# Performance work log

Hardware: AMD Instinct MI355X
Metric: run time of the kernel (lower is better)

The kernel has to match this reference:

```python
import jax, jax.numpy as jnp
import numpy as np
from jax import lax

B, C_IN, C, H, W = 4, 64, 64, 128, 128
K = 3  # window_size
SCALE = C ** (-0.5)
EPS = 1e-5  # BatchNorm eps (eval mode, running_mean=0, running_var=1)


def conv1x1(x, w, b):
    # x: (B,Ci,H,W), w: (Co,Ci)
    return jnp.einsum('bchw,oc->bohw', x, w) + b[None, :, None, None]


def unfold3(x):
    # torch nn.Unfold(kernel=3, pad=1, stride=1): (B,C,H,W) -> (B, C*9, H*W)
    b, c, h, w = x.shape
    xp = jnp.pad(x, ((0, 0), (0, 0), (1, 1), (1, 1)))
    patches = jnp.stack([xp[:, :, i:i + h, j:j + w]
                         for i in range(K) for j in range(K)], axis=2)  # (B,C,9,H,W)
    return patches.reshape(b, c * K * K, h * w)


def fold3(cols, h, w):
    # torch F.fold(kernel=3, pad=1, stride=1): (B, C*9, H*W) -> (B,C,H,W) scatter-add
    b = cols.shape[0]
    c = cols.shape[1] // (K * K)
    p = cols.reshape(b, c, K, K, h, w)
    out = jnp.zeros((b, c, h + 2, w + 2), cols.dtype)
    for i in range(K):
        for j in range(K):
            out = out.at[:, :, i:i + h, j:j + w].add(p[:, :, i, j])
    return out[:, :, 1:h + 1, 1:w + 1]


def grouped_conv3(x, w, groups):
    # 3x3 'same' conv with feature groups; w: (Cout, Cin/groups, 3, 3) OIHW
    return lax.conv_general_dilated(x, w, (1, 1), ((1, 1), (1, 1)),
                                    feature_group_count=groups,
                                    dimension_numbers=('NCHW', 'OIHW', 'NCHW'))


def bn_eval(x, g, b):
    # eval-mode BN with running_mean=0, running_var=1
    s = g / jnp.sqrt(1.0 + EPS)
    return x * s[None, :, None, None] + b[None, :, None, None]


def setup_inputs() -> dict:
    key = jax.random.key(0)
    ks = jax.random.split(key, 24)
    rn = lambda k, sh, s=1.0: (jax.random.normal(k, sh, dtype=jnp.float32) * s)
    return {
        'x':  rn(ks[0], (B, C_IN, H, W)),
        'fg': rn(ks[1], (B, C, H, W)),
        'bg': rn(ks[2], (B, C, H, W)),
        'w_x': rn(ks[3], (C, C_IN), 0.05), 'bias_x': rn(ks[4], (C,), 0.01),
        'w_f': rn(ks[5], (C, C), 0.05),    'bias_f': rn(ks[6], (C,), 0.01),
        'w_b': rn(ks[7], (C, C), 0.05),    'bias_b': rn(ks[8], (C,), 0.01),
        'w1': rn(ks[9], (C, 2, 3, 3), 0.1), 'b1': rn(ks[10], (C,), 0.01),
        'g1': jax.random.uniform(ks[11], (C,), dtype=jnp.float32, minval=0.5, maxval=1.5),
        'be1': rn(ks[12], (C,), 0.01),
        'w2': rn(ks[13], (C, C), 0.05), 'b2': rn(ks[14], (C,), 0.01),
        'w3': rn(ks[15], (C, 1, 3, 3), 0.1), 'b3': rn(ks[16], (C,), 0.01),
        'g2': jax.random.uniform(ks[17], (C,), dtype=jnp.float32, minval=0.5, maxval=1.5),
        'be2': rn(ks[18], (C,), 0.01),
        'w4': rn(ks[19], (C, C), 0.05), 'b4': rn(ks[20], (C,), 0.01),
    }


def reference(x, fg, bg, w_x, bias_x, w_f, bias_f, w_b, bias_b,
              w1, b1, g1, be1, w2, b2, w3, b3, g2, be2, w4, b4):
    b, _, h, w = x.shape
    xq  = conv1x1(x, w_x, bias_x)
    fgp = conv1x1(fg, w_f, bias_f)
    bgp = conv1x1(bg, w_b, bias_b)

    # unfold then the module's raw reshape (B, C*9, L) -> (B, C*L, 3, 3)
    xu = unfold3(xq).reshape(b, -1, K, K)
    fu = unfold3(fgp).reshape(b, -1, K, K)
    bu = unfold3(bgp).reshape(b, -1, K, K)

    attn_f = jax.nn.softmax(xu * fu, axis=-1) * xu * SCALE
    attn_b = jax.nn.softmax(xu - bu, axis=-1) * xu * SCALE

    # permute(0,2,3,1).view(B, 9*C, L) then fold back to (B,C,H,W)
    cols_f = attn_f.transpose(0, 2, 3, 1).reshape(b, K * K * C, -1)
    cols_b = attn_b.transpose(0, 2, 3, 1).reshape(b, K * K * C, -1)
    of = fold3(cols_f, h, w)
    ob = fold3(cols_b, h, w)

    a = jnp.concatenate([of, ob], axis=1)  # (B, 2C, H, W)
    y = grouped_conv3(a, w1, C) + b1[None, :, None, None]
    y = jax.nn.relu(bn_eval(y, g1, be1))
    y = conv1x1(y, w2, b2)
    y = grouped_conv3(y, w3, C) + b3[None, :, None, None]
    y = jax.nn.relu(bn_eval(y, g2, be2))
    y = conv1x1(y, w4, b4)
    return y
```

## Files before the change

### kernel.cpp

```cpp
#include <hip/hip_runtime.h>

#define NB 4
#define HWSZ 16384

typedef float f4u __attribute__((ext_vector_type(4), aligned(4)));
typedef _Float16 h8 __attribute__((ext_vector_type(8)));

#define PLANE_H ((size_t)1 << 21)

__device__ __forceinline__ void pw_body(int bid, int tid,
                                        const float* __restrict__ in,
                                        const float* __restrict__ w,
                                        const float* __restrict__ bias,
                                        float* __restrict__ out,
                                        float* wls) {
  int b = bid >> 8;
  int r = bid & 255;
  int oc = r >> 6;
  int pc = r & 63;
  int px4 = tid & 63;
  int og = tid >> 6;
  int px = (pc << 8) + (px4 << 2);
#pragma unroll
  for (int it = 0; it < 4; ++it)
    wls[(it << 8) + tid] = w[(oc << 10) + (it << 8) + tid];
  __syncthreads();
  int ob = (oc << 4) + (og << 2);
  float4 acc[4];
#pragma unroll
  for (int j = 0; j < 4; ++j) {
    float bv = bias[ob + j];
    acc[j] = make_float4(bv, bv, bv, bv);
  }
  const float* ip = in + (((size_t)b << 6) << 14) + px;
  const float* wp = wls + ((og << 2) << 6);
#pragma unroll 4
  for (int cc = 0; cc < 64; ++cc) {
    float4 xv = *(const float4*)(ip + ((size_t)cc << 14));
#pragma unroll
    for (int j = 0; j < 4; ++j) {
      float wv = wp[(j << 6) + cc];
      acc[j].x = fmaf(wv, xv.x, acc[j].x);
      acc[j].y = fmaf(wv, xv.y, acc[j].y);
      acc[j].z = fmaf(wv, xv.z, acc[j].z);
      acc[j].w = fmaf(wv, xv.w, acc[j].w);
    }
  }
#pragma unroll
  for (int j = 0; j < 4; ++j)
    *(float4*)(out + (((size_t)(b << 6) + ob + j) << 14) + px) = acc[j];
}

__global__ __launch_bounds__(256) void pw_k(const float* __restrict__ in,
                                            const float* __restrict__ w,
                                            const float* __restrict__ bias,
                                            float* __restrict__ out) {
  __shared__ float wls[16 * 64];
  pw_body(blockIdx.x, threadIdx.x, in, w, bias, out, wls);
}

__global__ __launch_bounds__(256) void pw3_k(const float* __restrict__ in0,
                                             const float* __restrict__ in1,
                                             const float* __restrict__ in2,
                                             const float* __restrict__ w0,
                                             const float* __restrict__ w1,
                                             const float* __restrict__ w2,
                                             const float* __restrict__ bi0,
                                             const float* __restrict__ bi1,
                                             const float* __restrict__ bi2,
                                             float* __restrict__ o0,
                                             float* __restrict__ o1,
                                             float* __restrict__ o2) {
  __shared__ float wls[16 * 64];
  int which = blockIdx.x >> 10;
  int bid = blockIdx.x & 1023;
  const float* in = (which == 0) ? in0 : (which == 1) ? in1 : in2;
  const float* w  = (which == 0) ? w0  : (which == 1) ? w1  : w2;
  const float* bi = (which == 0) ? bi0 : (which == 1) ? bi1 : bi2;
  float* out      = (which == 0) ? o0  : (which == 1) ? o1  : o2;
  pw_body(bid, threadIdx.x, in, w, bi, out, wls);
}

__global__ __launch_bounds__(256) void gconv1_k(const float* __restrict__ a,
                                                const float* __restrict__ w1,
                                                const float* __restrict__ b1,
                                                const float* __restrict__ g1,
                                                const float* __restrict__ be1,
                                                float* __restrict__ t1) {
  int bid = blockIdx.x;
  int b = bid >> 10;
  int r = bid & 1023;
  int o = r >> 4;
  int rc = r & 15;
  int tid = threadIdx.x;
  int px4 = tid & 31;
  int ry = tid >> 5;
  int y = (rc << 3) + ry;
  int x0 = px4 << 2;
  float bv = b1[o];
  float4 acc = make_float4(bv, bv, bv, bv);
#pragma unroll
  for (int ic = 0; ic < 2; ++ic) {
    const float* ap = a + ((size_t)(b * 128 + 2 * o + ic) << 14);
    const float* wr0 = w1 + o * 18 + ic * 9;
#pragma unroll
    for (int dy = 0; dy < 3; ++dy) {
      int yy = y + dy - 1;
      if ((unsigned)yy >= 128u) continue;
      const float* row = ap + (yy << 7);
      float4 mid = *(const float4*)(row + x0);
      float lf = (px4 > 0) ? row[x0 - 1] : 0.f;
      float rt = (px4 < 31) ? row[x0 + 4] : 0.f;
      float wa = wr0[dy * 3 + 0], wb = wr0[dy * 3 + 1], wc = wr0[dy * 3 + 2];
      acc.x += wa * lf    + wb * mid.x + wc * mid.y;
      acc.y += wa * mid.x + wb * mid.y + wc * mid.z;
      acc.z += wa * mid.y + wb * mid.z + wc * mid.w;
      acc.w += wa * mid.z + wb * mid.w + wc * rt;
    }
  }
  const float invs = 0.9999950000374997f;
  float s = g1[o] * invs, be = be1[o];
  acc.x = fmaxf(acc.x * s + be, 0.f);
  acc.y = fmaxf(acc.y * s + be, 0.f);
  acc.z = fmaxf(acc.z * s + be, 0.f);
  acc.w = fmaxf(acc.w * s + be, 0.f);
  *(float4*)(t1 + (((size_t)(b << 6) + o) << 14) + (y << 7) + x0) = acc;
}

__global__ __launch_bounds__(256) void dconv_k(const float* __restrict__ y2,
                                               const float* __restrict__ w3,
                                               const float* __restrict__ b3,
                                               const float* __restrict__ g2,
                                               const float* __restrict__ be2,
                                               float* __restrict__ t2) {
  int bid = blockIdx.x;
  int b = bid >> 10;
  int r = bid & 1023;
  int o = r >> 4;
  int rc = r & 15;
  int tid = threadIdx.x;
  int px4 = tid & 31;
  int ry = tid >> 5;
  int y = (rc << 3) + ry;
  int x0 = px4 << 2;
  float bv = b3[o];
  float4 acc = make_float4(bv, bv, bv, bv);
  const float* ap = y2 + (((size_t)(b << 6) + o) << 14);
  const float* wr0 = w3 + o * 9;
#pragma unroll
  for (int dy = 0; dy < 3; ++dy) {
    int yy = y + dy - 1;
    if ((unsigned)yy >= 128u) continue;
    const float* row = ap + (yy << 7);
    float4 mid = *(const float4*)(row + x0);
    float lf = (px4 > 0) ? row[x0 - 1] : 0.f;
    float rt = (px4 < 31) ? row[x0 + 4] : 0.f;
    float wa = wr0[dy * 3 + 0], wb = wr0[dy * 3 + 1], wc = wr0[dy * 3 + 2];
    acc.x += wa * lf    + wb * mid.x + wc * mid.y;
    acc.y += wa * mid.x + wb * mid.y + wc * mid.z;
    acc.z += wa * mid.y + wb * mid.z + wc * mid.w;
    acc.w += wa * mid.z + wb * mid.w + wc * rt;
  }
  const float invs = 0.9999950000374997f;
  float s = g2[o] * invs, be = be2[o];
  acc.x = fmaxf(acc.x * s + be, 0.f);
  acc.y = fmaxf(acc.y * s + be, 0.f);
  acc.z = fmaxf(acc.z * s + be, 0.f);
  acc.w = fmaxf(acc.w * s + be, 0.f);
  *(float4*)(t2 + (((size_t)(b << 6) + o) << 14) + (y << 7) + x0) = acc;
}

__global__ __launch_bounds__(256) void passA_k(const float* __restrict__ xq,
                                               const float* __restrict__ fgp,
                                               const float* __restrict__ bgp,
                                               _Float16* __restrict__ icols,
                                               int b0) {
  int bl = blockIdx.x >> 10;
  int vb = blockIdx.x & 1023;
  int v = ((vb & 7) << 7) + (vb >> 3);
  int n0 = ((v << 8) + threadIdx.x) << 2;
  int b = b0 + bl;
  const float* xqb = xq + ((size_t)b << 20);
  const float* fgb = fgp + ((size_t)b << 20);
  const float* bgb = bgp + ((size_t)b << 20);
  _Float16* ic = icols + (size_t)bl * 9 * PLANE_H;
  int c = n0 >> 14;
  int l0 = n0 & 16383;
  int t0 = 9 * l0;
  int r0 = t0 & 16383;
  int kk0 = t0 >> 14;
  float resF[9][4], resB[9][4];

  if (r0 <= 16348) {
    int ki = kk0 / 3, kj = kk0 - 3 * ki;
    int base0 = (c << 14) + r0 + ((ki - 1) << 7) + (kj - 1);
    int kj0 = (kj == 0), kj2 = (kj == 2), ki0 = (ki == 0), ki2 = (ki == 2);
#pragma unroll
    for (int q = 0; q < 4; ++q) {
      int hq = r0 + 9 * q;
      int xg0 = hq & 127, yg0 = hq >> 7;
      const float* px_ = xqb + base0 + 9 * q;
      const float* pf_ = fgb + base0 + 9 * q;
      const float* pb_ = bgb + base0 + 9 * q;
      f4u X0 = *(const f4u*)px_;
      f4u X1 = *(const f4u*)(px_ + 4);
      float X8 = px_[8];
      f4u F0 = *(const f4u*)pf_;
      f4u F1 = *(const f4u*)(pf_ + 4);
      float F8 = pf_[8];
      f4u B0 = *(const f4u*)pb_;
      f4u B1 = *(const f4u*)(pb_ + 4);
      float B8 = pb_[8];
      float XV[9], SF[9], SB[9];
#pragma unroll
      for (int e = 0; e < 9; ++e) {
        int xw = xg0 + e;
        int xp = xw & 127;
        int yp = yg0 + (xw >> 7);
        int inv = (kj0 & (xp == 0)) | (kj2 & (xp == 127)) |
                  (ki0 & (yp == 0)) | (ki2 & (yp == 127));
        float xv = (e < 4) ? X0[e] : ((e < 8) ? X1[e - 4] : X8);
        float fv = (e < 4) ? F0[e] : ((e < 8) ? F1[e - 4] : F8);
        float bv = (e < 4) ? B0[e] : ((e < 8) ? B1[e - 4] : B8);
        XV[e] = inv ? 0.f : xv;
        SF[e] = inv ? 0.f : xv * fv;
        SB[e] = inv ? 0.f : xv - bv;
      }
#pragma unroll
      for (int tr = 0; tr < 3; ++tr) {
        int e = 3 * tr;
        float mf = fmaxf(fmaxf(SF[e], SF[e + 1]), SF[e + 2]);
        float e0 = __expf(SF[e] - mf), e1 = __expf(SF[e + 1] - mf), e2 = __expf(SF[e + 2] - mf);
        float rs = 0.125f / (e0 + e1 + e2);
        resF[e + 0][q] = e0 * rs * XV[e + 0];
        resF[e + 1][q] = e1 * rs * XV[e + 1];
        resF[e + 2][q] = e2 * rs * XV[e + 2];
        float mb = fmaxf(fmaxf(SB[e], SB[e + 1]), SB[e + 2]);
        float g0 = __expf(SB[e] - mb), g1 = __expf(SB[e + 1] - mb), g2 = __expf(SB[e + 2] - mb);
        float rb = 0.125f / (g0 + g1 + g2);
        resB[e + 0][q] = g0 * rb * XV[e + 0];
        resB[e + 1][q] = g1 * rb * XV[e + 1];
        resB[e + 2][q] = g2 * rb * XV[e + 2];
      }
    }
  } else {
#pragma unroll
    for (int q = 0; q < 4; ++q) {
      float XV[9], SF[9], SB[9];
#pragma unroll
      for (int e = 0; e < 9; ++e) {
        int t = t0 + 9 * q + e;
        int kk = t >> 14;
        int hwp = t & 16383;
        int ki = kk / 3, kj = kk - 3 * ki;
        int sy = (hwp >> 7) + ki - 1;
        int sx = (hwp & 127) + kj - 1;
        float xv = 0.f, sf = 0.f, sb = 0.f;
        if (((unsigned)sy < 128u) && ((unsigned)sx < 128u)) {
          int off = (c << 14) + (sy << 7) + sx;
          xv = xqb[off];
          sf = xv * fgb[off];
          sb = xv - bgb[off];
        }
        XV[e] = xv; SF[e] = sf; SB[e] = sb;
      }
#pragma unroll
      for (int tr = 0; tr < 3; ++tr) {
        int e = 3 * tr;
        float mf = fmaxf(fmaxf(SF[e], SF[e + 1]), SF[e + 2]);
        float e0 = __expf(SF[e] - mf), e1 = __expf(SF[e + 1] - mf), e2 = __expf(SF[e + 2] - mf);
        float rs = 0.125f / (e0 + e1 + e2);
        resF[e + 0][q] = e0 * rs * XV[e + 0];
        resF[e + 1][q] = e1 * rs * XV[e + 1];
        resF[e + 2][q] = e2 * rs * XV[e + 2];
        float mb = fmaxf(fmaxf(SB[e], SB[e + 1]), SB[e + 2]);
        float g0 = __expf(SB[e] - mb), g1 = __expf(SB[e + 1] - mb), g2 = __expf(SB[e + 2] - mb);
        float rb = 0.125f / (g0 + g1 + g2);
        resB[e + 0][q] = g0 * rb * XV[e + 0];
        resB[e + 1][q] = g1 * rb * XV[e + 1];
        resB[e + 2][q] = g2 * rb * XV[e + 2];
      }
    }
  }
  size_t goff = (size_t)(n0 >> 2) << 3;
#pragma unroll
  for (int m = 0; m < 9; ++m) {
    h8 v;
    v[0] = (_Float16)resF[m][0]; v[1] = (_Float16)resF[m][1];
    v[2] = (_Float16)resF[m][2]; v[3] = (_Float16)resF[m][3];
    v[4] = (_Float16)resB[m][0]; v[5] = (_Float16)resB[m][1];
    v[6] = (_Float16)resB[m][2]; v[7] = (_Float16)resB[m][3];
    __builtin_nontemporal_store(v, (h8*)(ic + (size_t)m * PLANE_H + goff));
  }
}

__global__ __launch_bounds__(256) void passB_k(const _Float16* __restrict__ icols,
                                               float* __restrict__ a, int b0) {
  int bl = blockIdx.x >> 9;
  int idx = ((blockIdx.x & 511) << 8) + threadIdx.x;
  int b = b0 + bl;
  int c2 = idx >> 11;
  int hw0 = (idx << 3) & 16383;
  int y = hw0 >> 7, x0 = hw0 & 127;
  const _Float16* ic = icols + (size_t)bl * 9 * PLANE_H;
  float af[8], ab[8];
#pragma unroll
  for (int k = 0; k < 8; ++k) { af[k] = 0.f; ab[k] = 0.f; }
  h8 zero = {};
  int u9 = 9 * c2;
#pragma unroll
  for (int i = 0; i < 3; ++i) {
    int yp = y + 1 - i;
    if ((unsigned)yp >= 128u) continue;
#pragma unroll
    for (int j = 0; j < 3; ++j) {
      int u = u9 + 3 * i + j;
      int mp = u >> 6;
      int np = ((u & 63) << 14) + (yp << 7) + x0;
      const _Float16* p = ic + (size_t)mp * PLANE_H + ((size_t)np << 1);
      h8 G1 = __builtin_nontemporal_load((const h8*)p);
      h8 G2 = __builtin_nontemporal_load((const h8*)(p + 8));
      h8 G0 = (x0 > 0)   ? __builtin_nontemporal_load((const h8*)(p - 8))  : zero;
      h8 G3 = (x0 < 120) ? __builtin_nontemporal_load((const h8*)(p + 16)) : zero;
      float WF[10] = {(float)G0[3], (float)G1[0], (float)G1[1], (float)G1[2], (float)G1[3],
                      (float)G2[0], (float)G2[1], (float)G2[2], (float)G2[3], (float)G3[0]};
      float WB[10] = {(float)G0[7], (float)G1[4], (float)G1[5], (float)G1[6], (float)G1[7],
                      (float)G2[4], (float)G2[5], (float)G2[6], (float)G2[7], (float)G3[4]};
#pragma unroll
      for (int k = 0; k < 8; ++k) {
        af[k] += WF[k + 2 - j];
        ab[k] += WB[k + 2 - j];
      }
    }
  }
  float* aF = a + (((size_t)b * 128 + c2) << 14) + hw0;
  float* aB = a + (((size_t)b * 128 + 64 + c2) << 14) + hw0;
  *(float4*)(aF)     = make_float4(af[0], af[1], af[2], af[3]);
  *(float4*)(aF + 4) = make_float4(af[4], af[5], af[6], af[7]);
  *(float4*)(aB)     = make_float4(ab[0], ab[1], ab[2], ab[3]);
  *(float4*)(aB + 4) = make_float4(ab[4], ab[5], ab[6], ab[7]);
}

__device__ __forceinline__ void triel(const float* __restrict__ xqb,
                                      const float* __restrict__ fgb,
                                      const float* __restrict__ bgb,
                                      int fe, float& xv, float& sf, float& sb) {
  int u = fe >> 14;
  int hwp = fe & 16383;
  int c = u / 9;
  int kk = u - c * 9;
  int ki = kk / 3;
  int kj = kk - ki * 3;
  int sy = (hwp >> 7) + ki - 1;
  int sx = (hwp & 127) + kj - 1;
  if (((unsigned)sy < 128u) && ((unsigned)sx < 128u)) {
    int off = (c << 14) + (sy << 7) + sx;
    float xv_ = xqb[off];
    xv = xv_;
    sf = xv_ * fgb[off];
    sb = xv_ - bgb[off];
  } else {
    xv = 0.f; sf = 0.f; sb = 0.f;
  }
}

__global__ __launch_bounds__(256) void attnfold_k(const float* __restrict__ xq,
                                                  const float* __restrict__ fgp,
                                                  const float* __restrict__ bgp,
                                                  float* __restrict__ a) {
  int gidx = blockIdx.x * 256 + threadIdx.x;
  int hw = gidx & 16383;
  int bc = gidx >> 14;
  int c2 = bc & 63;
  int b = bc >> 6;
  int y = hw >> 7, x = hw & 127;
  const float* xqb = xq + (b << 20);
  const float* fgb = fgp + (b << 20);
  const float* bgb = bgp + (b << 20);
  float accf = 0.f, accb = 0.f;
#pragma unroll
  for (int i = 0; i < 3; ++i) {
    int yp = y + 1 - i;
    if ((unsigned)yp >= 128u) continue;
#pragma unroll
    for (int j = 0; j < 3; ++j) {
      int xp = x + 1 - j;
      if ((unsigned)xp >= 128u) continue;
      int g = ((c2 * 9 + i * 3 + j) << 14) + (yp << 7) + xp;
      int m = g >> 20;
      int n = g & 1048575;
      int f = n * 9 + m;
      int q = f % 3;
      int f0 = f - q;
      float xv0, sf0, sb0, xv1, sf1, sb1, xv2, sf2, sb2;
      triel(xqb, fgb, bgb, f0,     xv0, sf0, sb0);
      triel(xqb, fgb, bgb, f0 + 1, xv1, sf1, sb1);
      triel(xqb, fgb, bgb, f0 + 2, xv2, sf2, sb2);
      float xsel = (q == 0) ? xv0 : ((q == 1) ? xv1 : xv2);
      float mf = fmaxf(fmaxf(sf0, sf1), sf2);
      float ef0 = __expf(sf0 - mf), ef1 = __expf(sf1 - mf), ef2 = __expf(sf2 - mf);
      float self_f = (q == 0) ? ef0 : ((q == 1) ? ef1 : ef2);
      accf += self_f / (ef0 + ef1 + ef2) * xsel;
      float mb = fmaxf(fmaxf(sb0, sb1), sb2);
      float eb0 = __expf(sb0 - mb), eb1 = __expf(sb1 - mb), eb2 = __expf(sb2 - mb);
      float self_b = (q == 0) ? eb0 : ((q == 1) ? eb1 : eb2);
      accb += self_b / (eb0 + eb1 + eb2) * xsel;
    }
  }
  a[((b * 128 + c2) << 14) + hw] = accf * 0.125f;
  a[((b * 128 + 64 + c2) << 14) + hw] = accb * 0.125f;
}

extern "C" void kernel_launch(void* const* d_in, const int* in_sizes, int n_in,
                              void* d_out, int out_size, void* d_ws, size_t ws_size,
                              hipStream_t stream) {
  (void)in_sizes; (void)n_in; (void)out_size;
  const float* x      = (const float*)d_in[0];
  const float* fg     = (const float*)d_in[1];
  const float* bg     = (const float*)d_in[2];
  const float* w_x    = (const float*)d_in[3];
  const float* bias_x = (const float*)d_in[4];
  const float* w_f    = (const float*)d_in[5];
  const float* bias_f = (const float*)d_in[6];
  const float* w_b    = (const float*)d_in[7];
  const float* bias_b = (const float*)d_in[8];
  const float* w1     = (const float*)d_in[9];
  const float* b1     = (const float*)d_in[10];
  const float* g1     = (const float*)d_in[11];
  const float* be1    = (const float*)d_in[12];
  const float* w2     = (const float*)d_in[13];
  const float* b2     = (const float*)d_in[14];
  const float* w3     = (const float*)d_in[15];
  const float* b3     = (const float*)d_in[16];
  const float* g2     = (const float*)d_in[17];
  const float* be2    = (const float*)d_in[18];
  const float* w4     = (const float*)d_in[19];
  const float* b4     = (const float*)d_in[20];
  float* out = (float*)d_out;
  float* ws  = (float*)d_ws;

  const size_t NCHWf = (size_t)NB * 64 * HWSZ;
  float* base = ws + 256;
  float* xq  = base;
  float* fgp = base + NCHWf;
  float* bgp = base + 2 * NCHWf;
  float* a   = base + 3 * NCHWf;
  _Float16* icolsbase = (_Float16*)(base + 5 * NCHWf);
  float* t1 = fgp;
  float* y2 = xq;
  float* t2 = bgp;

  dim3 blk(256);
  pw3_k<<<3 * NB * 256, blk, 0, stream>>>(x, fg, bg, w_x, w_f, w_b,
                                          bias_x, bias_f, bias_b, xq, fgp, bgp);

  const size_t usedB = (5 * NCHWf + 512) * 4;
  const size_t perBatchColsB = 9 * PLANE_H * 2;
  size_t availB = (ws_size > usedB) ? (ws_size - usedB) : 0;
  int fit = (int)(availB / perBatchColsB);
  if (fit > NB) fit = NB;

  if (fit >= 1) {
    for (int b0 = 0; b0 < NB; b0 += fit) {
      int nb = (NB - b0 < fit) ? (NB - b0) : fit;
      passA_k<<<nb * 1024, blk, 0, stream>>>(xq, fgp, bgp, icolsbase, b0);
      passB_k<<<nb * 512, blk, 0, stream>>>(icolsbase, a, b0);
    }
  } else {
    attnfold_k<<<NB * 64 * HWSZ / 256, blk, 0, stream>>>(xq, fgp, bgp, a);
  }

  gconv1_k<<<NB * 1024, blk, 0, stream>>>(a, w1, b1, g1, be1, t1);
  pw_k<<<NB * 256, blk, 0, stream>>>(t1, w2, b2, y2);
  dconv_k<<<NB * 1024, blk, 0, stream>>>(y2, w3, b3, g2, be2, t2);
  pw_k<<<NB * 256, blk, 0, stream>>>(t2, w4, b4, out);
}
```

Baseline: 227.9 us.

## Interleave intermediate column planes per 64-thread group and simplify passA masking

Changes the fp16 intermediate buffer layout so that each 64-thread group writes its nine m-planes into one contiguous 4608-element chunk instead of nine planes spaced 2M elements apart. passB addressing is updated to read the same layout. The per-element boundary tests are replaced by a precomputed 9-bit mask, and the softmax division becomes a hardware reciprocal. Results are packed directly into fp16 vectors to cut register use. This aims to improve DRAM and cache locality of the writes and reduce ALU work, at the cost of slightly less precise normalization and possibly less contiguous access in passB.

```diff
diff --git a/kernel.cpp b/kernel.cpp
--- a/kernel.cpp
+++ b/kernel.cpp
@@ -178,7 +178,8 @@
   int bl = blockIdx.x >> 10;
   int vb = blockIdx.x & 1023;
   int v = ((vb & 7) << 7) + (vb >> 3);
-  int n0 = ((v << 8) + threadIdx.x) << 2;
+  int tid = threadIdx.x;
+  int n0 = ((v << 8) + tid) << 2;
   int b = b0 + bl;
   const float* xqb = xq + ((size_t)b << 20);
   const float* fgb = fgp + ((size_t)b << 20);
@@ -189,7 +190,7 @@
   int t0 = 9 * l0;
   int r0 = t0 & 16383;
   int kk0 = t0 >> 14;
-  float resF[9][4], resB[9][4];
+  h8 vout[9];
 
   if (r0 <= 16348) {
     int ki = kk0 / 3, kj = kk0 - 3 * ki;
@@ -199,6 +200,13 @@
     for (int q = 0; q < 4; ++q) {
       int hq = r0 + 9 * q;
       int xg0 = hq & 127, yg0 = hq >> 7;
+      int w0c = (xg0 >= 120) ? (128 - xg0) : 9;
+      int segA = (1 << w0c) - 1;
+      int rowA = (ki0 & (yg0 == 0)) | (ki2 & (yg0 == 127));
+      int rowB = ki2 & (yg0 == 126);
+      int mask9 = (rowA ? segA : 0) | (rowB ? (511 & ~segA) : 0);
+      mask9 |= kj0 ? ((xg0 == 0) ? 1 : ((xg0 >= 120) ? (1 << (128 - xg0)) : 0)) : 0;
+      mask9 |= kj2 ? ((xg0 >= 119) ? (1 << (127 - xg0)) : 0) : 0;
       const float* px_ = xqb + base0 + 9 * q;
       const float* pf_ = fgb + base0 + 9 * q;
       const float* pb_ = bgb + base0 + 9 * q;
@@ -214,33 +222,29 @@
       float XV[9], SF[9], SB[9];
 #pragma unroll
       for (int e = 0; e < 9; ++e) {
-        int xw = xg0 + e;
-        int xp = xw & 127;
-        int yp = yg0 + (xw >> 7);
-        int inv = (kj0 & (xp == 0)) | (kj2 & (xp == 127)) |
-                  (ki0 & (yp == 0)) | (ki2 & (yp == 127));
+        int iv = (mask9 >> e) & 1;
         float xv = (e < 4) ? X0[e] : ((e < 8) ? X1[e - 4] : X8);
         float fv = (e < 4) ? F0[e] : ((e < 8) ? F1[e - 4] : F8);
         float bv = (e < 4) ? B0[e] : ((e < 8) ? B1[e - 4] : B8);
-        XV[e] = inv ? 0.f : xv;
-        SF[e] = inv ? 0.f : xv * fv;
-        SB[e] = inv ? 0.f : xv - bv;
+        XV[e] = iv ? 0.f : xv;
+        SF[e] = iv ? 0.f : xv * fv;
+        SB[e] = iv ? 0.f : xv - bv;
       }
 #pragma unroll
       for (int tr = 0; tr < 3; ++tr) {
         int e = 3 * tr;
         float mf = fmaxf(fmaxf(SF[e], SF[e + 1]), SF[e + 2]);
         float e0 = __expf(SF[e] - mf), e1 = __expf(SF[e + 1] - mf), e2 = __expf(SF[e + 2] - mf);
-        float rs = 0.125f / (e0 + e1 + e2);
-        resF[e + 0][q] = e0 * rs * XV[e + 0];
-        resF[e + 1][q] = e1 * rs * XV[e + 1];
-        resF[e + 2][q] = e2 * rs * XV[e + 2];
+        float rs = __builtin_amdgcn_rcpf(e0 + e1 + e2) * 0.125f;
+        vout[e + 0][q] = (_Float16)(e0 * rs * XV[e + 0]);
+        vout[e + 1][q] = (_Float16)(e1 * rs * XV[e + 1]);
+        vout[e + 2][q] = (_Float16)(e2 * rs * XV[e + 2]);
         float mb = fmaxf(fmaxf(SB[e], SB[e + 1]), SB[e + 2]);
         float g0 = __expf(SB[e] - mb), g1 = __expf(SB[e + 1] - mb), g2 = __expf(SB[e + 2] - mb);
-        float rb = 0.125f / (g0 + g1 + g2);
-        resB[e + 0][q] = g0 * rb * XV[e + 0];
-        resB[e + 1][q] = g1 * rb * XV[e + 1];
-        resB[e + 2][q] = g2 * rb * XV[e + 2];
+        float rb = __builtin_amdgcn_rcpf(g0 + g1 + g2) * 0.125f;
+        vout[e + 0][4 + q] = (_Float16)(g0 * rb * XV[e + 0]);
+        vout[e + 1][4 + q] = (_Float16)(g1 * rb * XV[e + 1]);
+        vout[e + 2][4 + q] = (_Float16)(g2 * rb * XV[e + 2]);
       }
     }
   } else {
@@ -269,29 +273,23 @@
         int e = 3 * tr;
         float mf = fmaxf(fmaxf(SF[e], SF[e + 1]), SF[e + 2]);
         float e0 = __expf(SF[e] - mf), e1 = __expf(SF[e + 1] - mf), e2 = __expf(SF[e + 2] - mf);
-        float rs = 0.125f / (e0 + e1 + e2);
-        resF[e + 0][q] = e0 * rs * XV[e + 0];
-        resF[e + 1][q] = e1 * rs * XV[e + 1];
-        resF[e + 2][q] = e2 * rs * XV[e + 2];
+        float rs = __builtin_amdgcn_rcpf(e0 + e1 + e2) * 0.125f;
+        vout[e + 0][q] = (_Float16)(e0 * rs * XV[e + 0]);
+        vout[e + 1][q] = (_Float16)(e1 * rs * XV[e + 1]);
+        vout[e + 2][q] = (_Float16)(e2 * rs * XV[e + 2]);
         float mb = fmaxf(fmaxf(SB[e], SB[e + 1]), SB[e + 2]);
         float g0 = __expf(SB[e] - mb), g1 = __expf(SB[e + 1] - mb), g2 = __expf(SB[e + 2] - mb);
-        float rb = 0.125f / (g0 + g1 + g2);
-        resB[e + 0][q] = g0 * rb * XV[e + 0];
-        resB[e + 1][q] = g1 * rb * XV[e + 1];
-        resB[e + 2][q] = g2 * rb * XV[e + 2];
+        float rb = __builtin_amdgcn_rcpf(g0 + g1 + g2) * 0.125f;
+        vout[e + 0][4 + q] = (_Float16)(g0 * rb * XV[e + 0]);
+        vout[e + 1][4 + q] = (_Float16)(g1 * rb * XV[e + 1]);
+        vout[e + 2][4 + q] = (_Float16)(g2 * rb * XV[e + 2]);
       }
     }
   }
-  size_t goff = (size_t)(n0 >> 2) << 3;
-#pragma unroll
-  for (int m = 0; m < 9; ++m) {
-    h8 v;
-    v[0] = (_Float16)resF[m][0]; v[1] = (_Float16)resF[m][1];
-    v[2] = (_Float16)resF[m][2]; v[3] = (_Float16)resF[m][3];
-    v[4] = (_Float16)resB[m][0]; v[5] = (_Float16)resB[m][1];
-    v[6] = (_Float16)resB[m][2]; v[7] = (_Float16)resB[m][3];
-    __builtin_nontemporal_store(v, (h8*)(ic + (size_t)m * PLANE_H + goff));
-  }
+  size_t sbase = (size_t)(((v << 2) + (tid >> 6)) * 4608) + ((size_t)(tid & 63) << 3);
+#pragma unroll
+  for (int m = 0; m < 9; ++m)
+    __builtin_nontemporal_store(vout[m], (h8*)(ic + sbase + (size_t)m * 512));
 }
 
 __global__ __launch_bounds__(256) void passB_k(const _Float16* __restrict__ icols,
@@ -315,9 +313,9 @@
 #pragma unroll
     for (int j = 0; j < 3; ++j) {
       int u = u9 + 3 * i + j;
-      int mp = u >> 6;
-      int np = ((u & 63) << 14) + (yp << 7) + x0;
-      const _Float16* p = ic + (size_t)mp * PLANE_H + ((size_t)np << 1);
+      int mp = u >> 6, rem = u & 63;
+      int gp = (rem << 12) + (yp << 5) + (x0 >> 2);
+      const _Float16* p = ic + (size_t)(gp >> 6) * 4608 + mp * 512 + ((gp & 63) << 3);
       h8 G1 = __builtin_nontemporal_load((const h8*)p);
       h8 G2 = __builtin_nontemporal_load((const h8*)(p + 8));
       h8 G0 = (x0 > 0)   ? __builtin_nontemporal_load((const h8*)(p - 8))  : zero;
```

Result: slower. 256.4 us (+12.5%).
